# Performance work log

Hardware: AMD Instinct MI355X
Metric: run time of the kernel (lower is better)

## Reference

```python
import jax, jax.numpy as jnp
import numpy as np

N = 50000       # nodes
E = 1600000     # edges (avg degree 32)
D_IN = 128
HID = 64
HEADS = 2
D_OUT = 64
SLOPE = 0.2     # PyG GATConv default negative_slope


def setup_inputs() -> dict:
    key = jax.random.key(0)
    ks = jax.random.split(key, 10)
    s_in = 1.0 / np.sqrt(D_IN)
    s_h = 1.0 / np.sqrt(HEADS * HID)
    return {
        "x": jax.random.normal(ks[0], (N, D_IN), jnp.float32),
        "edge_index": jax.random.randint(ks[1], (2, E), 0, N, dtype=jnp.int64),
        "W1": jax.random.normal(ks[2], (D_IN, HEADS * HID), jnp.float32) * s_in,
        "att_src1": jax.random.normal(ks[3], (HEADS, HID), jnp.float32) * 0.1,
        "att_dst1": jax.random.normal(ks[4], (HEADS, HID), jnp.float32) * 0.1,
        "b1": jnp.zeros((HEADS * HID,), jnp.float32),
        "W2": jax.random.normal(ks[5], (HEADS * HID, D_OUT), jnp.float32) * s_h,
        "att_src2": jax.random.normal(ks[6], (1, D_OUT), jnp.float32) * 0.1,
        "att_dst2": jax.random.normal(ks[7], (1, D_OUT), jnp.float32) * 0.1,
        "b2": jnp.zeros((D_OUT,), jnp.float32),
    }


def gat_conv(x, W, a_src, a_dst, b, src, dst, num_nodes):
    """PyG GATConv (shared src/dst linear, self-loops already in src/dst), concat heads."""
    H, C = a_src.shape
    xp = (x @ W).reshape(num_nodes, H, C)          # [N,H,C]
    a_s = jnp.einsum('nhc,hc->nh', xp, a_src)       # [N,H]
    a_d = jnp.einsum('nhc,hc->nh', xp, a_dst)
    alpha = jax.nn.leaky_relu(a_s[src] + a_d[dst], SLOPE)          # [Etot,H]
    # numerically stable softmax over each destination neighborhood
    m = jax.ops.segment_max(alpha, dst, num_segments=num_nodes)     # [N,H]
    e = jnp.exp(alpha - m[dst])
    z = jax.ops.segment_sum(e, dst, num_segments=num_nodes)         # [N,H]
    coef = e / z[dst]                                               # [Etot,H]
    out = jax.ops.segment_sum(coef[:, :, None] * xp[src], dst, num_segments=num_nodes)  # [N,H,C]
    return out.reshape(num_nodes, H * C) + b


def reference(x, edge_index, W1, att_src1, att_dst1, b1, W2, att_src2, att_dst2, b2):
    loops = jnp.arange(N, dtype=edge_index.dtype)
    src = jnp.concatenate([edge_index[0], loops])   # add self-loops (PyG default)
    dst = jnp.concatenate([edge_index[1], loops])
    h = jax.nn.relu(gat_conv(x, W1, att_src1, att_dst1, b1, src, dst, N))
    return gat_conv(h, W2, att_src2, att_dst2, b2, src, dst, N)
```

## Files before the change

kernel.cpp:

```cpp
#include <hip/hip_runtime.h>
#include <hip/hip_bf16.h>
#include <hip/hip_fp16.h>


#define SLOPE 0.2f
static __device__ __forceinline__ float lrelu(float a) { return a > 0.f ? a : SLOPE * a; }

#define NBK_MAX 256

typedef _Float16 half8 __attribute__((ext_vector_type(8)));
typedef float f32x4 __attribute__((ext_vector_type(4)));


template <int K, int NOUT, int H, bool FUSE_BIN, int CHUNK, typename AT>
__global__ __launch_bounds__(256) void gemm_bin_mfma(
    const AT* __restrict__ A, const float* __restrict__ Wg,
    const float* __restrict__ att_s, const float* __restrict__ att_d,
    __half* __restrict__ Y, float* __restrict__ AS, float* __restrict__ AD,
    int M, int gemmBlocks,
    const int* __restrict__ srcArr, const int* __restrict__ dstArr,
    int* __restrict__ cursor, unsigned int* __restrict__ binned,
    int E2, int nbk, int capb) {
  constexpr int KK = K / 32;
  constexpr int NT = NOUT / 16;
  constexpr int NTH = NT / H;
  constexpr int LDW = K + 8;
  constexpr int LDY = NOUT + 8;
  constexpr int WTS_B = NOUT * LDW * 2;
  constexpr int YLDS_B = 4 * 16 * LDY * 2;
  constexpr int GEMM_B = (WTS_B > YLDS_B) ? WTS_B : YLDS_B;
  constexpr int BIN_B = 5 * 256 * 4 + CHUNK * 4;
  constexpr int SMEM_B = (FUSE_BIN && BIN_B > GEMM_B) ? BIN_B : GEMM_B;
  __shared__ __align__(16) char smem[SMEM_B];

  int tid = threadIdx.x;

  if constexpr (FUSE_BIN) {
    if ((int)blockIdx.x >= gemmBlocks) {
      int* hist = (int*)smem;
      int* lbase = hist + 256;
      int* lcur = lbase + 256;
      int* gpos = lcur + 256;
      int* sh = gpos + 256;
      unsigned int* stage = (unsigned int*)(sh + 256);
      constexpr int PT = CHUNK / 256;
      int t = tid;
      int bb = blockIdx.x - gemmBlocks;
      int e0 = bb * CHUNK;
      int cnt = min(CHUNK, E2 - e0);

      hist[t] = 0;
      __syncthreads();

      unsigned int pk[PT];
#pragma unroll
      for (int i = 0; i < PT; i++) {
        int e = e0 + t + i * 256;
        if (e < E2) {
          int s = srcArr[e], d = dstArr[e];
          int b = d >> 8;
          pk[i] = ((unsigned)b << 24) | ((unsigned)s << 8) | (unsigned)(d & 255);
          atomicAdd(&hist[b], 1);
        } else {
          pk[i] = 0xFFFFFFFFu;
        }
      }
      __syncthreads();

      int hv = hist[t];
      sh[t] = hv;
      __syncthreads();
      for (int o = 1; o < 256; o <<= 1) {
        int u = (t >= o) ? sh[t - o] : 0;
        __syncthreads();
        sh[t] += u;
        __syncthreads();
      }
      lbase[t] = sh[t] - hv;
      lcur[t] = sh[t] - hv;
      gpos[t] = hv ? (t * capb + atomicAdd(&cursor[t], hv)) : 0;
      __syncthreads();

#pragma unroll
      for (int i = 0; i < PT; i++) {
        if (pk[i] != 0xFFFFFFFFu) {
          int b = pk[i] >> 24;
          int lp = atomicAdd(&lcur[b], 1);
          stage[lp] = pk[i];
        }
      }
      __syncthreads();

      for (int i = t; i < cnt; i += 256) {
        unsigned int v = stage[i];
        int b = v >> 24;
        binned[gpos[b] + (i - lbase[b])] = v;
      }
      return;
    }
  }

  __half* wts = (__half*)smem;
  __half(*ylds)[16 * LDY] = (__half(*)[16 * LDY])smem;

  int w = tid >> 6;
  int lane = tid & 63;
  int lrow = lane & 15;
  int lch = lane >> 4;
  int r0w = blockIdx.x * 64 + w * 16;
  bool active = (r0w < M);

  for (int idx = tid; idx < NOUT * K; idx += 256) {
    int k = idx / NOUT, c = idx - k * NOUT;
    wts[c * LDW + k] = __float2half(Wg[idx]);
  }
  __syncthreads();

  f32x4 acc[NT];
#pragma unroll
  for (int nt = 0; nt < NT; nt++) acc[nt] = (f32x4){0.f, 0.f, 0.f, 0.f};

  if (active) {
    half8 afrag[KK];
    if constexpr (sizeof(AT) == 4) {
      const float* arow = (const float*)A + (size_t)(r0w + lrow) * K + lch * 8;
#pragma unroll
      for (int kk = 0; kk < KK; kk++) {
        float4 v0 = *(const float4*)(arow + kk * 32);
        float4 v1 = *(const float4*)(arow + kk * 32 + 4);
        half8 a;
        a[0] = (_Float16)v0.x; a[1] = (_Float16)v0.y;
        a[2] = (_Float16)v0.z; a[3] = (_Float16)v0.w;
        a[4] = (_Float16)v1.x; a[5] = (_Float16)v1.y;
        a[6] = (_Float16)v1.z; a[7] = (_Float16)v1.w;
        afrag[kk] = a;
      }
    } else {
      const __half* arow = (const __half*)A + (size_t)(r0w + lrow) * K + lch * 8;
#pragma unroll
      for (int kk = 0; kk < KK; kk++) afrag[kk] = *(const half8*)(arow + kk * 32);
    }

#pragma unroll
    for (int kk = 0; kk < KK; kk++) {
#pragma unroll
      for (int nt = 0; nt < NT; nt++) {
        half8 b = *(const half8*)&wts[(nt * 16 + lrow) * LDW + kk * 32 + lch * 8];
        acc[nt] = __builtin_amdgcn_mfma_f32_16x16x32_f16(afrag[kk], b, acc[nt], 0, 0, 0);
      }
    }

    float asw[NT], adw[NT];
#pragma unroll
    for (int nt = 0; nt < NT; nt++) {
      asw[nt] = att_s[nt * 16 + lrow];
      adw[nt] = att_d[nt * 16 + lrow];
    }
#pragma unroll
    for (int h = 0; h < H; h++) {
#pragma unroll
      for (int reg = 0; reg < 4; reg++) {
        float ps = 0.f, pd = 0.f;
#pragma unroll
        for (int nt = h * NTH; nt < (h + 1) * NTH; nt++) {
          ps = fmaf(acc[nt][reg], asw[nt], ps);
          pd = fmaf(acc[nt][reg], adw[nt], pd);
        }
#pragma unroll
        for (int o = 1; o < 16; o <<= 1) {
          ps += __shfl_xor(ps, o);
          pd += __shfl_xor(pd, o);
        }
        if (lrow == 0) {
          int row = r0w + lch * 4 + reg;
          AS[row * H + h] = ps;
          AD[row * H + h] = pd;
        }
      }
    }
  }

  __syncthreads();

  if (active) {
#pragma unroll
    for (int nt = 0; nt < NT; nt++) {
#pragma unroll
      for (int reg = 0; reg < 4; reg++) {
        ylds[w][(lch * 4 + reg) * LDY + nt * 16 + lrow] = __float2half(acc[nt][reg]);
      }
    }
  }
  __syncthreads();

  if (active) {
    constexpr int YCH = NOUT / 8;
    for (int idx = lane; idx < 16 * YCH; idx += 64) {
      int row = idx / YCH, ch = idx % YCH;
      uint4 v = *(const uint4*)&ylds[w][row * LDY + ch * 8];
      *(uint4*)(Y + (size_t)(r0w + row) * NOUT + ch * 8) = v;
    }
  }
}


template <int CAP>
__global__ void build_kernel(const unsigned int* __restrict__ binned,
                             const int* __restrict__ cursor, int* __restrict__ offsets,
                             int* __restrict__ csr_src, int Nn, int Etot, int nbk, int capb) {
  __shared__ int nhist[256];
  __shared__ int sh[256];
  __shared__ int lcur[256];
  __shared__ int sbase, ssz;
  __shared__ unsigned short stage[CAP];
  int b = blockIdx.x;
  int t = threadIdx.x;

  int gv = (t < nbk) ? cursor[t] : 0;
  sh[t] = gv;
  __syncthreads();
  for (int o = 1; o < 256; o <<= 1) {
    int u = (t >= o) ? sh[t - o] : 0;
    __syncthreads();
    sh[t] += u;
    __syncthreads();
  }
  if (t == b) { sbase = sh[t] - gv; ssz = gv; }
  __syncthreads();
  int csrbase = sbase;
  int sz = ssz;
  int binbase = b * capb;

  nhist[t] = 0;
  __syncthreads();
  for (int i = t; i < sz; i += 256) atomicAdd(&nhist[binned[binbase + i] & 255], 1);
  __syncthreads();

  int hv = nhist[t];
  sh[t] = hv;
  __syncthreads();
  for (int o = 1; o < 256; o <<= 1) {
    int u = (t >= o) ? sh[t - o] : 0;
    __syncthreads();
    sh[t] += u;
    __syncthreads();
  }
  int excl = sh[t] - hv;
  int node = (b << 8) + t;
  if (node < Nn) offsets[node] = csrbase + excl;
  if (b == nbk - 1 && t == 0) offsets[Nn] = Etot;
  lcur[t] = excl;
  __syncthreads();

  if (sz <= CAP) {
    for (int i = t; i < sz; i += 256) {
      unsigned int v = binned[binbase + i];
      int lp = atomicAdd(&lcur[v & 255], 1);
      stage[lp] = (unsigned short)((v >> 8) & 0xFFFFu);
    }
    __syncthreads();
    for (int i = t; i < sz; i += 256) csr_src[csrbase + i] = (int)stage[i];
  } else {
    for (int i = t; i < sz; i += 256) {
      unsigned int v = binned[binbase + i];
      int lp = atomicAdd(&lcur[v & 255], 1);
      csr_src[csrbase + lp] = (int)((v >> 8) & 0xFFFFu);
    }
  }
}


static __device__ __forceinline__ void fma8(uint4 u, float e, float* __restrict__ acc) {
  float2 f0 = __half22float2(*(const __half2*)&u.x);
  float2 f1 = __half22float2(*(((const __half2*)&u.x) + 1));
  float2 f2 = __half22float2(*(const __half2*)&u.z);
  float2 f3 = __half22float2(*(((const __half2*)&u.z) + 1));
  acc[0] = fmaf(e, f0.x, acc[0]); acc[1] = fmaf(e, f0.y, acc[1]);
  acc[2] = fmaf(e, f1.x, acc[2]); acc[3] = fmaf(e, f1.y, acc[3]);
  acc[4] = fmaf(e, f2.x, acc[4]); acc[5] = fmaf(e, f2.y, acc[5]);
  acc[6] = fmaf(e, f3.x, acc[6]); acc[7] = fmaf(e, f3.y, acc[7]);
}

static __device__ __forceinline__ void pk4(uint4 u, unsigned ep, __half2* __restrict__ acc2) {
  __half2 e2 = *(const __half2*)&ep;
  acc2[0] = __hfma2(e2, *(const __half2*)&u.x, acc2[0]);
  acc2[1] = __hfma2(e2, *(((const __half2*)&u.x) + 1), acc2[1]);
  acc2[2] = __hfma2(e2, *(const __half2*)&u.z, acc2[2]);
  acc2[3] = __hfma2(e2, *(((const __half2*)&u.z) + 1), acc2[3]);
}

template <int H, bool RELU, typename OT>
__global__ void node_kernel(const int* __restrict__ offsets, const int* __restrict__ csr_src,
                            const float* __restrict__ AS, const float* __restrict__ AD,
                            const __half* __restrict__ XPH, const float* __restrict__ bias,
                            OT* __restrict__ OUT, int Nn) {
  constexpr int ROWH = H * 64;
  constexpr int LPE = (H == 2) ? 16 : 8;
  constexpr int G = 64 / LPE;
  int n = blockIdx.x;
  int lane = threadIdx.x & 63;
  int g = lane / LPE;
  int sub = lane & (LPE - 1);

  int beg = offsets[n], end = offsets[n + 1];
  int deg = end - beg;

  const __half* base = XPH + sub * 8;

  float acc[8];
#pragma unroll
  for (int k = 0; k < 8; k++) acc[k] = 0.f;
  float z0 = 0.f, z1 = 0.f;

  float ad0, ad1 = 0.f;
  if constexpr (H == 2) {
    float2 adn = ((const float2*)AD)[n];
    ad0 = adn.x; ad1 = adn.y;
  } else {
    ad0 = AD[n];
  }

  if constexpr (H == 2) {
    float2 asn = ((const float2*)AS)[n];
    float es0 = __expf(lrelu(asn.x + ad0));
    float es1 = __expf(lrelu(asn.y + ad1));
    if (g == 0) {
      uint4 u = *(const uint4*)(base + (size_t)n * ROWH);
      fma8(u, (lane & 8) ? es1 : es0, acc);
    }
    if (lane == 0) { z0 = es0; z1 = es1; }
  } else {
    float es = __expf(lrelu(AS[n] + ad0));
    if (g == 0) {
      uint4 u = *(const uint4*)(base + (size_t)n * ROWH);
      fma8(u, es, acc);
    }
    if (lane == 0) z0 = es;
  }

  for (int i0 = 0; i0 < deg; i0 += 64) {
    int cnt = min(64, deg - i0);
    int srcv = 0;
    int epk = 0;
    float ev0 = 0.f, ev1 = 0.f;
    if (lane < cnt) {
      srcv = csr_src[beg + i0 + lane];
      if constexpr (H == 2) {
        float2 asv = ((const float2*)AS)[srcv];
        ev0 = __expf(lrelu(asv.x + ad0));
        ev1 = __expf(lrelu(asv.y + ad1));
        __half h0 = __float2half(ev0), h1 = __float2half(ev1);
        epk = (int)(((unsigned)*(unsigned short*)&h1 << 16) | *(unsigned short*)&h0);
      } else {
        ev0 = __expf(lrelu(AS[srcv] + ad0));
        __half h0 = __float2half(ev0);
        unsigned short us = *(unsigned short*)&h0;
        epk = (int)(((unsigned)us << 16) | us);
      }
    }
    z0 += ev0;
    if constexpr (H == 2) z1 += ev1;

    auto sel = [&](int p) -> unsigned {
      unsigned short us;
      if constexpr (H == 2)
        us = (lane & 8) ? (unsigned short)((unsigned)p >> 16) : (unsigned short)((unsigned)p & 0xFFFFu);
      else
        us = (unsigned short)((unsigned)p & 0xFFFFu);
      return ((unsigned)us << 16) | us;
    };

    int j = 0;
    for (; j + 4 * G <= cnt; j += 4 * G) {
      int s0 = __shfl(srcv, j + g),         s1 = __shfl(srcv, j + G + g);
      int s2 = __shfl(srcv, j + 2 * G + g), s3 = __shfl(srcv, j + 3 * G + g);
      int p0 = __shfl(epk, j + g),          p1 = __shfl(epk, j + G + g);
      int p2 = __shfl(epk, j + 2 * G + g),  p3 = __shfl(epk, j + 3 * G + g);
      uint4 u0 = *(const uint4*)(base + (size_t)s0 * ROWH);
      uint4 u1 = *(const uint4*)(base + (size_t)s1 * ROWH);
      uint4 u2 = *(const uint4*)(base + (size_t)s2 * ROWH);
      uint4 u3 = *(const uint4*)(base + (size_t)s3 * ROWH);
      __half2 acc2[4];
      acc2[0] = __half2(__half(0.f), __half(0.f));
      acc2[1] = acc2[0]; acc2[2] = acc2[0]; acc2[3] = acc2[0];
      pk4(u0, sel(p0), acc2);
      pk4(u1, sel(p1), acc2);
      pk4(u2, sel(p2), acc2);
      pk4(u3, sel(p3), acc2);
#pragma unroll
      for (int k = 0; k < 4; k++) {
        float2 f = __half22float2(acc2[k]);
        acc[2 * k] += f.x;
        acc[2 * k + 1] += f.y;
      }
    }
    for (; j + G <= cnt; j += G) {
      int s = __shfl(srcv, j + g);
      int p = __shfl(epk, j + g);
      __half_raw hr; hr.x = (unsigned short)(sel(p) & 0xFFFFu);
      float e = __half2float(__half(hr));
      uint4 u = *(const uint4*)(base + (size_t)s * ROWH);
      fma8(u, e, acc);
    }
    if (j < cnt) {
      int idx = j + g;
      int s = __shfl(srcv, idx & 63);
      int p = __shfl(epk, idx & 63);
      if (idx < cnt) {
        __half_raw hr; hr.x = (unsigned short)(sel(p) & 0xFFFFu);
        float e = __half2float(__half(hr));
        uint4 u = *(const uint4*)(base + (size_t)s * ROWH);
        fma8(u, e, acc);
      }
    }
  }

#pragma unroll
  for (int o = LPE; o <= 32; o <<= 1) {
#pragma unroll
    for (int k = 0; k < 8; k++) acc[k] += __shfl_xor(acc[k], o);
  }
  for (int o = 32; o > 0; o >>= 1) {
    z0 += __shfl_xor(z0, o);
    if constexpr (H == 2) z1 += __shfl_xor(z1, o);
  }
  float inv;
  if constexpr (H == 2) inv = 1.0f / ((lane & 8) ? z1 : z0);
  else inv = 1.0f / z0;

  if (g == 0) {
    const float* bp = bias + sub * 8;
    float r[8];
#pragma unroll
    for (int k = 0; k < 8; k++) {
      r[k] = fmaf(acc[k], inv, bp[k]);
      if (RELU) r[k] = fmaxf(r[k], 0.f);
    }
    if constexpr (sizeof(OT) == 4) {
      float* op = (float*)OUT + (size_t)n * ROWH + sub * 8;
      ((float4*)op)[0] = make_float4(r[0], r[1], r[2], r[3]);
      ((float4*)op)[1] = make_float4(r[4], r[5], r[6], r[7]);
    } else {
      __half* op = (__half*)OUT + (size_t)n * ROWH + sub * 8;
      __half2 h0 = __floats2half2_rn(r[0], r[1]);
      __half2 h1 = __floats2half2_rn(r[2], r[3]);
      __half2 h2 = __floats2half2_rn(r[4], r[5]);
      __half2 h3 = __floats2half2_rn(r[6], r[7]);
      uint4 u;
      u.x = *(unsigned int*)&h0; u.y = *(unsigned int*)&h1;
      u.z = *(unsigned int*)&h2; u.w = *(unsigned int*)&h3;
      *(uint4*)op = u;
    }
  }
}


static inline size_t alignup(size_t x) { return (x + 255) & ~(size_t)255; }

extern "C" void kernel_launch(void* const* d_in, const int* in_sizes, int n_in,
                              void* d_out, int out_size, void* d_ws, size_t ws_size,
                              hipStream_t stream) {
  const float* x    = (const float*)d_in[0];
  const int*   edges= (const int*)d_in[1];
  const float* W1   = (const float*)d_in[2];
  const float* as1w = (const float*)d_in[3];
  const float* ad1w = (const float*)d_in[4];
  const float* b1   = (const float*)d_in[5];
  const float* W2   = (const float*)d_in[6];
  const float* as2w = (const float*)d_in[7];
  const float* ad2w = (const float*)d_in[8];
  const float* b2   = (const float*)d_in[9];

  const int N = in_sizes[0] / 128;
  const int E = in_sizes[1] / 2;
  const int* src = edges;
  const int* dst = edges + E;
  const int nbk = (N + 255) >> 8;

  constexpr int CHUNK = 2048;
  constexpr int CAPB = 10240;

  char* p = (char*)d_ws;
  size_t off = 0;
  auto take = [&](size_t bytes) { char* r = p + off; off = alignup(off + bytes); return r; };
  __half* xph1 = (__half*)take((size_t)N * 128 * 2);
  __half* xph2 = (__half*)take((size_t)N * 64 * 2);
  __half* hbuf = (__half*)take((size_t)N * 128 * 2);
  float* as1   = (float*)take((size_t)N * 2 * 4);
  float* ad1   = (float*)take((size_t)N * 2 * 4);
  float* as2   = (float*)take((size_t)N * 4);
  float* ad2   = (float*)take((size_t)N * 4);
  int* offsets = (int*)take((size_t)(N + 1) * 4);
  int* csr_src = (int*)take((size_t)E * 4);
  unsigned int* binned = (unsigned int*)take((size_t)nbk * CAPB * 4);
  int* cursor  = (int*)take((size_t)NBK_MAX * 4);
  (void)ws_size;

  const int binBlocks = (E + CHUNK - 1) / CHUNK;
  const int gemmBlocks = (N + 63) / 64;

  hipMemsetAsync(cursor, 0, (size_t)NBK_MAX * 4, stream);

  gemm_bin_mfma<128, 128, 2, true, CHUNK, float><<<gemmBlocks + binBlocks, 256, 0, stream>>>(
      x, W1, as1w, ad1w, xph1, as1, ad1, N, gemmBlocks,
      src, dst, cursor, binned, E, nbk, CAPB);

  build_kernel<12288><<<nbk, 256, 0, stream>>>(binned, cursor, offsets, csr_src, N, E, nbk, CAPB);

  node_kernel<2, true, __half><<<N, 64, 0, stream>>>(
      offsets, csr_src, as1, ad1, xph1, b1, hbuf, N);

  gemm_bin_mfma<128, 64, 1, false, CHUNK, __half><<<gemmBlocks, 256, 0, stream>>>(
      hbuf, W2, as2w, ad2w, xph2, as2, ad2, N, gemmBlocks,
      nullptr, nullptr, nullptr, nullptr, 0, nbk, CAPB);
  node_kernel<1, false, float><<<N, 64, 0, stream>>>(
      offsets, csr_src, as2, ad2, xph2, b2, (float*)d_out, N);
}
```

Before: 143.5 us.

## Fold layer-2 attention projections into layer-1 node epilogue; split GEMM weight staging

Precomputes W2·att_src2 and W2·att_dst2 as 128-element vectors in an extra block of the first fused kernel. The layer-1 aggregation epilogue then computes the layer-2 attention logits directly from the fp32 post-ReLU activations, so the second GEMM skips its attention reduction. The GEMM also stages weights into shared memory in two K halves, which shrinks the LDS footprint to raise occupancy at the cost of an extra barrier pair. The layer-2 logits now come from fp32 activations rather than the fp16-rounded GEMM output, which can shift numerics slightly.

Result: slower. 152.8 us (+6.5%).

```diff
diff --git a/kernel.cpp b/kernel.cpp
--- a/kernel.cpp
+++ b/kernel.cpp
@@ -12,7 +12,7 @@
 typedef float f32x4 __attribute__((ext_vector_type(4)));
 
 
-template <int K, int NOUT, int H, bool FUSE_BIN, int CHUNK, typename AT>
+template <int K, int NOUT, int H, bool FUSE_BIN, bool DO_ATT, int CHUNK, typename AT>
 __global__ __launch_bounds__(256) void gemm_bin_mfma(
     const AT* __restrict__ A, const float* __restrict__ Wg,
     const float* __restrict__ att_s, const float* __restrict__ att_d,
@@ -20,11 +20,13 @@
     int M, int gemmBlocks,
     const int* __restrict__ srcArr, const int* __restrict__ dstArr,
     int* __restrict__ cursor, unsigned int* __restrict__ binned,
-    int E2, int nbk, int capb) {
-  constexpr int KK = K / 32;
+    int E2, int nbk, int capb,
+    const float* __restrict__ W2g, const float* __restrict__ as2wg,
+    const float* __restrict__ ad2wg, float* __restrict__ vs2, float* __restrict__ vd2) {
   constexpr int NT = NOUT / 16;
   constexpr int NTH = NT / H;
-  constexpr int LDW = K + 8;
+  constexpr int KH = 64;
+  constexpr int LDW = KH + 8;
   constexpr int LDY = NOUT + 8;
   constexpr int WTS_B = NOUT * LDW * 2;
   constexpr int YLDS_B = 4 * 16 * LDY * 2;
@@ -36,6 +38,19 @@
   int tid = threadIdx.x;
 
   if constexpr (FUSE_BIN) {
+    if ((int)blockIdx.x == (int)gridDim.x - 1) {
+      for (int c = tid; c < 128; c += 256) {
+        float s = 0.f, d = 0.f;
+        for (int j = 0; j < 64; j++) {
+          float w = W2g[c * 64 + j];
+          s = fmaf(w, as2wg[j], s);
+          d = fmaf(w, ad2wg[j], d);
+        }
+        vs2[c] = s;
+        vd2[c] = d;
+      }
+      return;
+    }
     if ((int)blockIdx.x >= gemmBlocks) {
       int* hist = (int*)smem;
       int* lbase = hist + 256;
@@ -110,22 +125,16 @@
   int r0w = blockIdx.x * 64 + w * 16;
   bool active = (r0w < M);
 
-  for (int idx = tid; idx < NOUT * K; idx += 256) {
-    int k = idx / NOUT, c = idx - k * NOUT;
-    wts[c * LDW + k] = __float2half(Wg[idx]);
-  }
-  __syncthreads();
-
   f32x4 acc[NT];
 #pragma unroll
   for (int nt = 0; nt < NT; nt++) acc[nt] = (f32x4){0.f, 0.f, 0.f, 0.f};
 
+  half8 afrag[K / 32];
   if (active) {
-    half8 afrag[KK];
     if constexpr (sizeof(AT) == 4) {
       const float* arow = (const float*)A + (size_t)(r0w + lrow) * K + lch * 8;
 #pragma unroll
-      for (int kk = 0; kk < KK; kk++) {
+      for (int kk = 0; kk < K / 32; kk++) {
         float4 v0 = *(const float4*)(arow + kk * 32);
         float4 v1 = *(const float4*)(arow + kk * 32 + 4);
         half8 a;
@@ -138,18 +147,31 @@
     } else {
       const __half* arow = (const __half*)A + (size_t)(r0w + lrow) * K + lch * 8;
 #pragma unroll
-      for (int kk = 0; kk < KK; kk++) afrag[kk] = *(const half8*)(arow + kk * 32);
-    }
-
-#pragma unroll
-    for (int kk = 0; kk < KK; kk++) {
-#pragma unroll
-      for (int nt = 0; nt < NT; nt++) {
-        half8 b = *(const half8*)&wts[(nt * 16 + lrow) * LDW + kk * 32 + lch * 8];
-        acc[nt] = __builtin_amdgcn_mfma_f32_16x16x32_f16(afrag[kk], b, acc[nt], 0, 0, 0);
-      }
-    }
-
+      for (int kk = 0; kk < K / 32; kk++) afrag[kk] = *(const half8*)(arow + kk * 32);
+    }
+  }
+
+#pragma unroll
+  for (int ph = 0; ph < 2; ph++) {
+    for (int idx = tid; idx < NOUT * KH; idx += 256) {
+      int kl = idx / NOUT, c = idx - kl * NOUT;
+      wts[c * LDW + kl] = __float2half(Wg[(ph * KH + kl) * NOUT + c]);
+    }
+    __syncthreads();
+    if (active) {
+#pragma unroll
+      for (int kk = 0; kk < 2; kk++) {
+#pragma unroll
+        for (int nt = 0; nt < NT; nt++) {
+          half8 b = *(const half8*)&wts[(nt * 16 + lrow) * LDW + kk * 32 + lch * 8];
+          acc[nt] = __builtin_amdgcn_mfma_f32_16x16x32_f16(afrag[ph * 2 + kk], b, acc[nt], 0, 0, 0);
+        }
+      }
+    }
+    __syncthreads();
+  }
+
+  if (DO_ATT && active) {
     float asw[NT], adw[NT];
 #pragma unroll
     for (int nt = 0; nt < NT; nt++) {
@@ -179,8 +201,6 @@
       }
     }
   }
-
-  __syncthreads();
 
   if (active) {
 #pragma unroll
@@ -289,11 +309,13 @@
   acc2[3] = __hfma2(e2, *(((const __half2*)&u.z) + 1), acc2[3]);
 }
 
-template <int H, bool RELU, typename OT>
+template <int H, bool RELU, bool FATT2, typename OT>
 __global__ void node_kernel(const int* __restrict__ offsets, const int* __restrict__ csr_src,
                             const float* __restrict__ AS, const float* __restrict__ AD,
                             const __half* __restrict__ XPH, const float* __restrict__ bias,
-                            OT* __restrict__ OUT, int Nn) {
+                            OT* __restrict__ OUT, int Nn,
+                            const float* __restrict__ vs2, const float* __restrict__ vd2,
+                            float* __restrict__ as2o, float* __restrict__ ad2o) {
   constexpr int ROWH = H * 64;
   constexpr int LPE = (H == 2) ? 16 : 8;
   constexpr int G = 64 / LPE;
@@ -436,6 +458,20 @@
       r[k] = fmaf(acc[k], inv, bp[k]);
       if (RELU) r[k] = fmaxf(r[k], 0.f);
     }
+    if constexpr (FATT2) {
+      float ps = 0.f, pd = 0.f;
+#pragma unroll
+      for (int k = 0; k < 8; k++) {
+        ps = fmaf(r[k], vs2[sub * 8 + k], ps);
+        pd = fmaf(r[k], vd2[sub * 8 + k], pd);
+      }
+#pragma unroll
+      for (int o = 1; o < 16; o <<= 1) {
+        ps += __shfl_xor(ps, o);
+        pd += __shfl_xor(pd, o);
+      }
+      if (lane == 0) { as2o[n] = ps; ad2o[n] = pd; }
+    }
     if constexpr (sizeof(OT) == 4) {
       float* op = (float*)OUT + (size_t)n * ROWH + sub * 8;
       ((float4*)op)[0] = make_float4(r[0], r[1], r[2], r[3]);
@@ -490,6 +526,8 @@
   float* ad1   = (float*)take((size_t)N * 2 * 4);
   float* as2   = (float*)take((size_t)N * 4);
   float* ad2   = (float*)take((size_t)N * 4);
+  float* vs2   = (float*)take(128 * 4);
+  float* vd2   = (float*)take(128 * 4);
   int* offsets = (int*)take((size_t)(N + 1) * 4);
   int* csr_src = (int*)take((size_t)E * 4);
   unsigned int* binned = (unsigned int*)take((size_t)nbk * CAPB * 4);
@@ -501,18 +539,22 @@
 
   hipMemsetAsync(cursor, 0, (size_t)NBK_MAX * 4, stream);
 
-  gemm_bin_mfma<128, 128, 2, true, CHUNK, float><<<gemmBlocks + binBlocks, 256, 0, stream>>>(
+  gemm_bin_mfma<128, 128, 2, true, true, CHUNK, float>
+      <<<gemmBlocks + binBlocks + 1, 256, 0, stream>>>(
       x, W1, as1w, ad1w, xph1, as1, ad1, N, gemmBlocks,
-      src, dst, cursor, binned, E, nbk, CAPB);
+      src, dst, cursor, binned, E, nbk, CAPB,
+      W2, as2w, ad2w, vs2, vd2);
 
   build_kernel<12288><<<nbk, 256, 0, stream>>>(binned, cursor, offsets, csr_src, N, E, nbk, CAPB);
 
-  node_kernel<2, true, __half><<<N, 64, 0, stream>>>(
-      offsets, csr_src, as1, ad1, xph1, b1, hbuf, N);
-
-  gemm_bin_mfma<128, 64, 1, false, CHUNK, __half><<<gemmBlocks, 256, 0, stream>>>(
+  node_kernel<2, true, true, __half><<<N, 64, 0, stream>>>(
+      offsets, csr_src, as1, ad1, xph1, b1, hbuf, N, vs2, vd2, as2, ad2);
+
+  gemm_bin_mfma<128, 64, 1, false, false, CHUNK, __half><<<gemmBlocks, 256, 0, stream>>>(
       hbuf, W2, as2w, ad2w, xph2, as2, ad2, N, gemmBlocks,
-      nullptr, nullptr, nullptr, nullptr, 0, nbk, CAPB);
-  node_kernel<1, false, float><<<N, 64, 0, stream>>>(
-      offsets, csr_src, as2, ad2, xph2, b2, (float*)d_out, N);
+      nullptr, nullptr, nullptr, nullptr, 0, nbk, CAPB,
+      nullptr, nullptr, nullptr, nullptr, nullptr);
+  node_kernel<1, false, false, float><<<N, 64, 0, stream>>>(
+      offsets, csr_src, as2, ad2, xph2, b2, (float*)d_out, N,
+      nullptr, nullptr, nullptr, nullptr);
 }
```
